# Performance work log

Hardware: AMD Instinct MI355X
Metric: run time of the kernel (lower is better)

## Reference

```python
import jax, jax.numpy as jnp
import numpy as np

H = 256        # hidden_size
HEADS = 8      # conv1 heads
B = 256        # number of graphs (sessions)
L = 64         # nodes per graph (max_length)
N = B * L      # total nodes
E = 131072     # edges before self-loops
NNODE = 37000  # item vocabulary / num classes


def setup_inputs() -> dict:
    key = jax.random.key(0)
    ks = jax.random.split(key, 16)
    s = 0.02
    return {
        "x_ids": jax.random.randint(ks[0], (N,), 0, NNODE + 1),
        "edge_index": jax.random.randint(ks[1], (2, E), 0, N),
        "batch": jnp.repeat(jnp.arange(B, dtype=jnp.int32), L),
        "emb": jax.random.normal(ks[2], (NNODE + 1, H)) * s,
        "W1": jax.random.normal(ks[3], (H, HEADS * H)) * s,
        "att_src1": jax.random.normal(ks[4], (HEADS, H)) * s,
        "att_dst1": jax.random.normal(ks[5], (HEADS, H)) * s,
        "b1": jnp.zeros((HEADS * H,)),
        "W2": jax.random.normal(ks[6], (HEADS * H, H)) * s,
        "att_src2": jax.random.normal(ks[7], (1, H)) * s,
        "att_dst2": jax.random.normal(ks[8], (1, H)) * s,
        "b2": jnp.zeros((H,)),
        "Wih": jax.random.normal(ks[9], (4 * H, H)) * s,
        "Whh": jax.random.normal(ks[10], (4 * H, H)) * s,
        "bih": jnp.zeros((4 * H,)),
        "bhh": jnp.zeros((4 * H,)),
        "Wp": jax.random.normal(ks[11], (NNODE, H)) * s,
        "bp": jnp.zeros((NNODE,)),
    }


def gat_conv(x, src, dst, W, a_src, a_dst, bias, concat):
    # PyG GATConv: linear -> per-head attention logits -> leaky_relu ->
    # segment-softmax over incoming edges per dst node -> scatter-add.
    n = x.shape[0]
    heads = a_src.shape[0]
    h = (x @ W).reshape(n, heads, -1)                       # [N, heads, out]
    alpha_s = (h * a_src).sum(-1)                            # [N, heads]
    alpha_d = (h * a_dst).sum(-1)
    e = jax.nn.leaky_relu(alpha_s[src] + alpha_d[dst], 0.2)  # [E, heads]
    m = jax.ops.segment_max(e, dst, num_segments=n)
    p = jnp.exp(e - m[dst])
    z = jax.ops.segment_sum(p, dst, num_segments=n)
    alpha = p / (z[dst] + 1e-16)                             # edge softmax
    out = jax.ops.segment_sum(alpha[:, :, None] * h[src], dst, num_segments=n)
    out = out.reshape(n, -1) if concat else out.mean(axis=1)
    return out + bias


def reference(x_ids, edge_index, batch, emb, W1, att_src1, att_dst1, b1,
              W2, att_src2, att_dst2, b2, Wih, Whh, bih, bhh, Wp, bp):
    n = x_ids.shape[0]
    # GATConv default add_self_loops=True
    loops = jnp.arange(n)
    src = jnp.concatenate([edge_index[0], loops])
    dst = jnp.concatenate([edge_index[1], loops])

    emb = emb.at[0].set(0.0)  # padding_idx=0
    x = emb[x_ids]
    # eval mode: dropout is identity
    x = jax.nn.elu(gat_conv(x, src, dst, W1, att_src1, att_dst1, b1, True))
    x = gat_conv(x, src, dst, W2, att_src2, att_dst2, b2, False)  # [N, H]

    # pack variable-length graphs into padded [B, L, H] sequences
    lengths = jax.ops.segment_sum(jnp.ones((n,), jnp.int32), batch, num_segments=B)
    starts = jnp.cumsum(lengths) - lengths
    pos = jnp.arange(n) - starts[batch]
    seq = jnp.zeros((B, L, x.shape[-1]), x.dtype).at[batch, pos].set(x)
    mask = jnp.arange(L)[None, :] < lengths[:, None]  # [B, L]

    # single-layer LSTM; masking emulates pack_padded_sequence: h_n is the
    # hidden state at each sequence's true last timestep
    def step(carry, xs):
        h_prev, c_prev = carry
        x_t, m_t = xs
        g = x_t @ Wih.T + h_prev @ Whh.T + bih + bhh
        i, f, gg, o = jnp.split(g, 4, axis=-1)
        c_new = jax.nn.sigmoid(f) * c_prev + jax.nn.sigmoid(i) * jnp.tanh(gg)
        h_new = jax.nn.sigmoid(o) * jnp.tanh(c_new)
        mm = m_t[:, None]
        return (jnp.where(mm, h_new, h_prev), jnp.where(mm, c_new, c_prev)), None

    h0 = jnp.zeros((B, x.shape[-1]), x.dtype)
    (hT, _), _ = jax.lax.scan(step, (h0, h0),
                              (seq.transpose(1, 0, 2), mask.T))
    return hT @ Wp.T + bp  # [B, NNODE] scores
```

## Files before the change

### kernel.cpp

```cpp
#include <hip/hip_runtime.h>
#include <hip/hip_bf16.h>
#include <cstdint>

#define HD 256
#define NHEADS 8
#define NB 256
#define SL 64
#define NN 16384
#define NE 131072
#define NTOT (NE + NN)

typedef float floatx4 __attribute__((ext_vector_type(4)));
typedef short shortx8 __attribute__((ext_vector_type(8)));
typedef unsigned short ushortx8 __attribute__((ext_vector_type(8)));
typedef unsigned short ushortx4 __attribute__((ext_vector_type(4)));

__device__ __forceinline__ unsigned short f2bf(float f) {
    union { float f; unsigned u; } a; a.f = f;
    unsigned r = a.u + 0x7fffu + ((a.u >> 16) & 1u);
    return (unsigned short)(r >> 16);
}
__device__ __forceinline__ float bf2f(unsigned short b) {
    union { unsigned u; float f; } a; a.u = ((unsigned)b) << 16;
    return a.f;
}

__device__ __forceinline__ void store_b16_sys(unsigned short* p, unsigned v) {
    asm volatile("global_store_short %0, %1, off sc0 sc1" :: "v"(p), "v"(v) : "memory");
}
__device__ __forceinline__ shortx8 load_b128_sys(const unsigned short* p) {
    shortx8 r;
    asm volatile("global_load_dwordx4 %0, %1, off sc0 sc1" : "=v"(r) : "v"(p) : "memory");
    return r;
}


__global__ void k_cast_bf16(const float* __restrict__ in, unsigned short* __restrict__ out, int n4) {
    int i = blockIdx.x * 256 + threadIdx.x;
    if (i >= n4) return;
    float4 v = ((const float4*)in)[i];
    ushortx4 o;
    o[0] = f2bf(v.x); o[1] = f2bf(v.y); o[2] = f2bf(v.z); o[3] = f2bf(v.w);
    *(ushortx4*)&out[i * 4] = o;
}

__global__ void k_transpose_bf16(const float* __restrict__ in, unsigned short* __restrict__ out,
                                 int K, int N) {
    __shared__ float t[32][33];
    int nb = blockIdx.x * 32, kb = blockIdx.y * 32;
    int tx = threadIdx.x, ty = threadIdx.y;
#pragma unroll
    for (int i = 0; i < 4; ++i) {
        int k = kb + ty + i * 8;
        t[ty + i * 8][tx] = in[(size_t)k * N + nb + tx];
    }
    __syncthreads();
#pragma unroll
    for (int i = 0; i < 4; ++i) {
        int nrow = nb + ty + i * 8;
        out[(size_t)nrow * K + kb + tx] = f2bf(t[tx][ty + i * 8]);
    }
}

__global__ void k_add2(const float* __restrict__ a, const float* __restrict__ b,
                       float* __restrict__ o, int n) {
    int i = blockIdx.x * 256 + threadIdx.x;
    if (i < n) o[i] = a[i] + b[i];
}

__global__ void k_zero(int* __restrict__ p, int n) {
    int i = blockIdx.x * 256 + threadIdx.x;
    if (i < n) p[i] = 0;
}

__global__ void k_gather_x(const int* __restrict__ ids, const float* __restrict__ emb,
                           unsigned short* __restrict__ xb) {
    int i = blockIdx.x * 256 + threadIdx.x;
    int n = i >> 6, d4 = (i & 63) << 2;
    int id = ids[n];
    float4 v = make_float4(0.f, 0.f, 0.f, 0.f);
    if (id != 0) v = *(const float4*)&emb[(size_t)id * HD + d4];
    ushortx4 o;
    o[0] = f2bf(v.x); o[1] = f2bf(v.y); o[2] = f2bf(v.z); o[3] = f2bf(v.w);
    *(ushortx4*)&xb[(size_t)n * HD + d4] = o;
}


template <bool OUT_BF16, bool HAS_BIAS>
__global__ __launch_bounds__(256, 2) void k_gemm_bt(
    const unsigned short* __restrict__ A, const unsigned short* __restrict__ B,
    void* __restrict__ C, const float* __restrict__ bias, int M, int Nn, int K) {
    constexpr int LDT = 56;
    __shared__ unsigned short As[128 * LDT];
    __shared__ unsigned short Bs[128 * LDT];
    int tid = threadIdx.x;
    int wave = tid >> 6, lane = tid & 63;
    int q = lane >> 4, c16 = lane & 15;
    long m0 = (long)blockIdx.x * 128;
    long n0 = (long)blockIdx.y * 128;
    int wm = (wave & 1) << 6, wn = (wave >> 1) << 6;
    floatx4 acc[4][4] = {};
    int lrow = tid >> 2;
    int lk = (tid & 3) << 3;
    const unsigned short* Arow0 = A + (m0 + lrow) * K + lk;
    const unsigned short* Arow1 = A + (m0 + 64 + lrow) * K + lk;
    long nb0 = n0 + lrow;      if (nb0 >= Nn) nb0 = Nn - 1;
    long nb1 = n0 + 64 + lrow; if (nb1 >= Nn) nb1 = Nn - 1;
    const unsigned short* Brow0 = B + nb0 * K + lk;
    const unsigned short* Brow1 = B + nb1 * K + lk;

    for (int k0 = 0; k0 < K; k0 += 32) {
        ushortx8 a0 = *(const ushortx8*)(Arow0 + k0);
        ushortx8 a1 = *(const ushortx8*)(Arow1 + k0);
        ushortx8 b0 = *(const ushortx8*)(Brow0 + k0);
        ushortx8 b1 = *(const ushortx8*)(Brow1 + k0);
        __syncthreads();
        *(ushortx8*)&As[lrow * LDT + lk] = a0;
        *(ushortx8*)&As[(64 + lrow) * LDT + lk] = a1;
        *(ushortx8*)&Bs[lrow * LDT + lk] = b0;
        *(ushortx8*)&Bs[(64 + lrow) * LDT + lk] = b1;
        __syncthreads();
        shortx8 af[4], bfr[4];
#pragma unroll
        for (int mt = 0; mt < 4; ++mt)
            af[mt] = *(const shortx8*)&As[(wm + mt * 16 + c16) * LDT + q * 8];
#pragma unroll
        for (int nt = 0; nt < 4; ++nt)
            bfr[nt] = *(const shortx8*)&Bs[(wn + nt * 16 + c16) * LDT + q * 8];
#pragma unroll
        for (int mt = 0; mt < 4; ++mt)
#pragma unroll
            for (int nt = 0; nt < 4; ++nt)
                acc[mt][nt] = __builtin_amdgcn_mfma_f32_16x16x32_bf16(af[mt], bfr[nt], acc[mt][nt], 0, 0, 0);
    }
#pragma unroll
    for (int mt = 0; mt < 4; ++mt) {
        long row_base = m0 + wm + mt * 16 + q * 4;
#pragma unroll
        for (int nt = 0; nt < 4; ++nt) {
            long col = n0 + wn + nt * 16 + c16;
            if (col >= Nn) continue;
            float bv = HAS_BIAS ? bias[col] : 0.0f;
#pragma unroll
            for (int r = 0; r < 4; ++r) {
                float v = acc[mt][nt][r] + bv;
                long idx = (row_base + r) * (long)Nn + col;
                if (OUT_BF16) ((unsigned short*)C)[idx] = f2bf(v);
                else          ((float*)C)[idx] = v;
            }
        }
    }
}


__global__ void k_alpha1(const unsigned short* __restrict__ h1b, const float* __restrict__ asrc,
                         const float* __restrict__ adst, float* __restrict__ als,
                         float* __restrict__ ald) {
    int n = blockIdx.x, t = threadIdx.x;
    ushortx8 hv = *(const ushortx8*)&h1b[(size_t)n * 2048 + t * 8];
    float s = 0.f, d = 0.f;
#pragma unroll
    for (int j = 0; j < 8; ++j) {
        float f = bf2f(hv[j]);
        s += f * asrc[t * 8 + j];
        d += f * adst[t * 8 + j];
    }
    for (int o = 16; o; o >>= 1) { s += __shfl_down(s, o, 32); d += __shfl_down(d, o, 32); }
    if ((t & 31) == 0) { als[n * 8 + (t >> 5)] = s; ald[n * 8 + (t >> 5)] = d; }
}

__global__ void k_alpha2(const unsigned short* __restrict__ x2b, const float* __restrict__ asrc,
                         const float* __restrict__ adst, float* __restrict__ als,
                         float* __restrict__ ald) {
    int n = blockIdx.x, t = threadIdx.x;
    ushortx4 hv = *(const ushortx4*)&x2b[(size_t)n * 256 + t * 4];
    float s = 0.f, d = 0.f;
#pragma unroll
    for (int j = 0; j < 4; ++j) {
        float f = bf2f(hv[j]);
        s += f * asrc[t * 4 + j];
        d += f * adst[t * 4 + j];
    }
    for (int o = 32; o; o >>= 1) { s += __shfl_down(s, o, 64); d += __shfl_down(d, o, 64); }
    if (t == 0) { als[n] = s; ald[n] = d; }
}


__global__ void k_deg_init(int* __restrict__ deg) {
    int i = blockIdx.x * 256 + threadIdx.x;
    if (i < NN) deg[i] = 1;
}
__global__ void k_deg_count(const int* __restrict__ ei, int* __restrict__ deg) {
    int e = blockIdx.x * 256 + threadIdx.x;
    if (e < NE) atomicAdd(&deg[ei[NE + e]], 1);
}
__global__ void k_scan(const int* __restrict__ deg, int* __restrict__ row_start,
                       int* __restrict__ cursor) {
    __shared__ int s[1024];
    int t = threadIdx.x;
    int base = t * 16;
    int loc[16]; int sum = 0;
#pragma unroll
    for (int i = 0; i < 16; ++i) { loc[i] = deg[base + i]; sum += loc[i]; }
    s[t] = sum;
    __syncthreads();
    for (int o = 1; o < 1024; o <<= 1) {
        int v = (t >= o) ? s[t - o] : 0;
        __syncthreads();
        s[t] += v;
        __syncthreads();
    }
    int ex = s[t] - sum;
#pragma unroll
    for (int i = 0; i < 16; ++i) {
        row_start[base + i] = ex;
        cursor[base + i] = ex;
        ex += loc[i];
    }
    if (t == 0) row_start[NN] = NTOT;
}
__global__ void k_fill(const int* __restrict__ ei, int* __restrict__ cursor,
                       int* __restrict__ csr_src) {
    int e = blockIdx.x * 256 + threadIdx.x;
    if (e >= NTOT) return;
    int s, d;
    if (e < NE) { s = ei[e]; d = ei[NE + e]; }
    else        { s = e - NE; d = s; }
    int p = atomicAdd(&cursor[d], 1);
    csr_src[p] = s;
}


__global__ __launch_bounds__(256) void k_agg1(
    const int* __restrict__ row_start, const int* __restrict__ csr_src,
    const float* __restrict__ als, const float* __restrict__ ald,
    const unsigned short* __restrict__ h1b, const float* __restrict__ b1,
    unsigned short* __restrict__ out1b) {
    int n = blockIdx.x, t = threadIdx.x;
    int rs = row_start[n];
    int deg = row_start[n + 1] - rs;
    __shared__ float sm[8], sz[8], sad[8];
    if (t < 8) sad[t] = ald[n * 8 + t];
    __syncthreads();
    int hh = t >> 5, ii = t & 31;
    float adh = sad[hh];
    float lm = -1e30f;
    for (int i = ii; i < deg; i += 32) {
        int s = csr_src[rs + i];
        float e = als[s * 8 + hh] + adh;
        e = e >= 0.f ? e : 0.2f * e;
        lm = fmaxf(lm, e);
    }
    for (int o = 16; o; o >>= 1) lm = fmaxf(lm, __shfl_down(lm, o, 32));
    if (ii == 0) sm[hh] = lm;
    __syncthreads();
    float mh = sm[hh];
    float lz = 0.f;
    for (int i = ii; i < deg; i += 32) {
        int s = csr_src[rs + i];
        float e = als[s * 8 + hh] + adh;
        e = e >= 0.f ? e : 0.2f * e;
        lz += expf(e - mh);
    }
    for (int o = 16; o; o >>= 1) lz += __shfl_down(lz, o, 32);
    if (ii == 0) sz[hh] = lz;
    __syncthreads();
    float inv_z = 1.0f / (sz[hh] + 1e-16f);
    float acc[8] = {0.f, 0.f, 0.f, 0.f, 0.f, 0.f, 0.f, 0.f};
    for (int i = 0; i < deg; ++i) {
        int s = csr_src[rs + i];
        float e = als[s * 8 + hh] + adh;
        e = e >= 0.f ? e : 0.2f * e;
        float w = expf(e - mh) * inv_z;
        ushortx8 hv = *(const ushortx8*)&h1b[(size_t)s * 2048 + t * 8];
#pragma unroll
        for (int j = 0; j < 8; ++j) acc[j] += w * bf2f(hv[j]);
    }
    ushortx8 o8;
#pragma unroll
    for (int j = 0; j < 8; ++j) {
        float v = acc[j] + b1[t * 8 + j];
        v = v > 0.f ? v : expm1f(v);
        o8[j] = f2bf(v);
    }
    *(ushortx8*)&out1b[(size_t)n * 2048 + t * 8] = o8;
}

__global__ void k_agg2(const int* __restrict__ row_start, const int* __restrict__ csr_src,
                       const float* __restrict__ als, const float* __restrict__ ald,
                       const unsigned short* __restrict__ x2b, const float* __restrict__ b2,
                       unsigned short* __restrict__ out2b) {
    int n = blockIdx.x, t = threadIdx.x;
    int rs = row_start[n];
    int deg = row_start[n + 1] - rs;
    float adn = ald[n];
    float lm = -1e30f;
    for (int i = t; i < deg; i += 64) {
        float e = als[csr_src[rs + i]] + adn;
        e = e >= 0.f ? e : 0.2f * e;
        lm = fmaxf(lm, e);
    }
    for (int o = 32; o; o >>= 1) lm = fmaxf(lm, __shfl_down(lm, o, 64));
    float mh = __shfl(lm, 0, 64);
    float lz = 0.f;
    for (int i = t; i < deg; i += 64) {
        float e = als[csr_src[rs + i]] + adn;
        e = e >= 0.f ? e : 0.2f * e;
        lz += expf(e - mh);
    }
    for (int o = 32; o; o >>= 1) lz += __shfl_down(lz, o, 64);
    float zz = __shfl(lz, 0, 64);
    float inv_z = 1.0f / (zz + 1e-16f);
    float acc[4] = {0.f, 0.f, 0.f, 0.f};
    for (int i = 0; i < deg; ++i) {
        int s = csr_src[rs + i];
        float e = als[s] + adn;
        e = e >= 0.f ? e : 0.2f * e;
        float w = expf(e - mh) * inv_z;
        ushortx4 hv = *(const ushortx4*)&x2b[(size_t)s * 256 + t * 4];
#pragma unroll
        for (int j = 0; j < 4; ++j) acc[j] += w * bf2f(hv[j]);
    }
    ushortx4 o4;
#pragma unroll
    for (int j = 0; j < 4; ++j) o4[j] = f2bf(acc[j] + b2[t * 4 + j]);
    *(ushortx4*)&out2b[(size_t)n * 256 + t * 4] = o4;
}

__global__ void k_repack_whh(const unsigned short* __restrict__ Whhb,
                             unsigned short* __restrict__ WhhR) {
    int i = blockIdx.x * 256 + threadIdx.x;
    int lane = i & 63;
    int fi = i >> 6;
    int f = fi & 3, k0 = (fi >> 2) & 7, w = (fi >> 5) & 3, s = fi >> 7;
    int q = lane >> 4, c16 = lane & 15;
    int gcol = f * 256 + s * 64 + w * 16 + c16;
    int k = k0 * 32 + q * 8;
    ushortx8 v = *(const ushortx8*)&Whhb[(size_t)gcol * 256 + k];
    *(ushortx8*)&WhhR[(size_t)fi * 512 + lane * 8] = v;
}


__global__ __launch_bounds__(256, 1) void k_lstm8(
    const float* __restrict__ Xg, const unsigned short* __restrict__ WhhR,
    unsigned short* __restrict__ hX, int* __restrict__ flags) {
    __shared__ unsigned short wlds[4 * 32 * 512];

    int tid = threadIdx.x;
    int w = tid >> 6, lane = tid & 63;
    int q = lane >> 4, c16 = lane & 15;
    int g = blockIdx.x & 15, s = blockIdx.x >> 4;
    int scol = s * 64 + w * 16 + c16;
    const int fbase = g * 64;

    const unsigned short* wsrc = WhhR + (size_t)((s * 4 + w) * 32) * 512 + lane * 8;
#pragma unroll
    for (int fi = 0; fi < 32; ++fi)
        *(shortx8*)&wlds[(w * 32 + fi) * 512 + lane * 8] =
            *(const shortx8*)(wsrc + fi * 512);

    float cst[4] = {0.f, 0.f, 0.f, 0.f};

    for (int t = 0; t < SL; ++t) {
        float xg[4][4];
#pragma unroll
        for (int r = 0; r < 4; ++r) {
            const float* xp = Xg + ((size_t)(g * 16 + q * 4 + r) * SL + t) * 1024 + scol;
#pragma unroll
            for (int f = 0; f < 4; ++f) xg[r][f] = xp[f * 256];
        }

        floatx4 acc[4] = {};
        if (t > 0) {
            if (tid == 0) {
                int spins = 0;
                while (__hip_atomic_fetch_add(&flags[fbase + t - 1], 0, __ATOMIC_RELAXED,
                                              __HIP_MEMORY_SCOPE_AGENT) < 4) {
                    __builtin_amdgcn_s_sleep(2);
                    if (++spins > 65536) break;
                }
            }
            __syncthreads();

            const unsigned short* hp =
                hX + ((size_t)(t - 1) * 256 + g * 16 + c16) * 256 + q * 8;
            shortx8 af[8];
#pragma unroll
            for (int k0 = 0; k0 < 8; ++k0) af[k0] = load_b128_sys(hp + k0 * 32);
            asm volatile("s_waitcnt vmcnt(0)" ::: "memory");
            __builtin_amdgcn_sched_barrier(0);
#pragma unroll
            for (int k0 = 0; k0 < 8; ++k0)
#pragma unroll
                for (int f = 0; f < 4; ++f) {
                    shortx8 b = *(const shortx8*)&wlds[(w * 32 + k0 * 4 + f) * 512 + lane * 8];
                    acc[f] = __builtin_amdgcn_mfma_f32_16x16x32_bf16(af[k0], b, acc[f], 0, 0, 0);
                }
        }

        unsigned short* hw = hX + ((size_t)t * 256 + g * 16) * 256 + scol;
#pragma unroll
        for (int r = 0; r < 4; ++r) {
            float gi = acc[0][r] + xg[r][0];
            float gf = acc[1][r] + xg[r][1];
            float gG = acc[2][r] + xg[r][2];
            float go = acc[3][r] + xg[r][3];
            float si = __builtin_amdgcn_rcpf(1.f + __expf(-gi));
            float sf = __builtin_amdgcn_rcpf(1.f + __expf(-gf));
            float so = __builtin_amdgcn_rcpf(1.f + __expf(-go));
            float tg = 1.f - 2.f * __builtin_amdgcn_rcpf(1.f + __expf(2.f * gG));
            float c = sf * cst[r] + si * tg;
            cst[r] = c;
            float tc = 1.f - 2.f * __builtin_amdgcn_rcpf(1.f + __expf(2.f * c));
            store_b16_sys(hw + (q * 4 + r) * 256, (unsigned)f2bf(so * tc));
        }

        if (t < SL - 1) {
            asm volatile("s_waitcnt vmcnt(0)" ::: "memory");
            __syncthreads();
            if (tid == 0)
                __hip_atomic_fetch_add(&flags[fbase + t], 1, __ATOMIC_RELAXED,
                                       __HIP_MEMORY_SCOPE_AGENT);
        }
    }
}


extern "C" void kernel_launch(void* const* d_in, const int* in_sizes, int n_in,
                              void* d_out, int out_size, void* d_ws, size_t ws_size,
                              hipStream_t stream) {
    const int*   x_ids = (const int*)d_in[0];
    const int*   ei    = (const int*)d_in[1];
    const float* emb   = (const float*)d_in[3];
    const float* W1    = (const float*)d_in[4];
    const float* as1w  = (const float*)d_in[5];
    const float* ad1w  = (const float*)d_in[6];
    const float* b1    = (const float*)d_in[7];
    const float* W2    = (const float*)d_in[8];
    const float* as2w  = (const float*)d_in[9];
    const float* ad2w  = (const float*)d_in[10];
    const float* b2    = (const float*)d_in[11];
    const float* Wih   = (const float*)d_in[12];
    const float* Whh   = (const float*)d_in[13];
    const float* bih   = (const float*)d_in[14];
    const float* bhh   = (const float*)d_in[15];
    const float* Wp    = (const float*)d_in[16];
    const float* bp    = (const float*)d_in[17];

    char* ws = (char*)d_ws;
    size_t off = 0;
    auto alloc = [&](size_t bytes) -> void* {
        void* p = ws + off;
        off += (bytes + 255) & ~(size_t)255;
        return p;
    };
    unsigned short* h1b   = (unsigned short*)alloc((size_t)NN * 2048 * 2);
    float*          Xg    = (float*)h1b;
    unsigned short* out1b = (unsigned short*)alloc((size_t)NN * 2048 * 2);
    unsigned short* hX    = out1b;
    unsigned short* xb    = (unsigned short*)alloc((size_t)NN * 256 * 2);
    unsigned short* x2b   = (unsigned short*)alloc((size_t)NN * 256 * 2);
    unsigned short* out2b = (unsigned short*)alloc((size_t)NN * 256 * 2);
    unsigned short* W1t   = (unsigned short*)alloc((size_t)2048 * 256 * 2);
    unsigned short* W2t   = (unsigned short*)alloc((size_t)256 * 2048 * 2);
    unsigned short* Wihb  = (unsigned short*)alloc((size_t)1024 * 256 * 2);
    unsigned short* Whhb  = (unsigned short*)alloc((size_t)1024 * 256 * 2);
    unsigned short* WhhR  = (unsigned short*)alloc((size_t)1024 * 256 * 2);
    unsigned short* Wpb   = (unsigned short*)alloc((size_t)37000 * 256 * 2);
    float*          bb    = (float*)alloc(1024 * 4);
    float*          als1  = (float*)alloc((size_t)NN * 8 * 4);
    float*          ald1  = (float*)alloc((size_t)NN * 8 * 4);
    float*          als2  = (float*)alloc((size_t)NN * 4);
    float*          ald2  = (float*)alloc((size_t)NN * 4);
    int* deg       = (int*)alloc((size_t)NN * 4);
    int* row_start = (int*)alloc((size_t)(NN + 1) * 4);
    int* cursor    = (int*)alloc((size_t)NN * 4);
    int* csr_src   = (int*)alloc((size_t)NTOT * 4);
    int* flags     = (int*)alloc((size_t)16 * 64 * 4);
    (void)ws_size; (void)in_sizes; (void)n_in; (void)out_size;

    k_transpose_bf16<<<dim3(2048 / 32, 256 / 32), dim3(32, 8), 0, stream>>>(W1, W1t, 256, 2048);
    k_transpose_bf16<<<dim3(256 / 32, 2048 / 32), dim3(32, 8), 0, stream>>>(W2, W2t, 2048, 256);
    k_cast_bf16<<<(262144 / 4 + 255) / 256, 256, 0, stream>>>(Wih, Wihb, 262144 / 4);
    k_cast_bf16<<<(262144 / 4 + 255) / 256, 256, 0, stream>>>(Whh, Whhb, 262144 / 4);
    k_cast_bf16<<<(9472000 / 4 + 255) / 256, 256, 0, stream>>>(Wp, Wpb, 9472000 / 4);
    k_add2<<<4, 256, 0, stream>>>(bih, bhh, bb, 1024);
    k_repack_whh<<<32768 / 256, 256, 0, stream>>>(Whhb, WhhR);
    k_zero<<<4, 256, 0, stream>>>(flags, 1024);

    k_deg_init<<<NN / 256, 256, 0, stream>>>(deg);
    k_deg_count<<<NE / 256, 256, 0, stream>>>(ei, deg);
    k_scan<<<1, 1024, 0, stream>>>(deg, row_start, cursor);
    k_fill<<<(NTOT + 255) / 256, 256, 0, stream>>>(ei, cursor, csr_src);

    k_gather_x<<<NN * 64 / 256, 256, 0, stream>>>(x_ids, emb, xb);

    k_gemm_bt<true, false><<<dim3(NN / 128, 2048 / 128), 256, 0, stream>>>(
        xb, W1t, h1b, nullptr, NN, 2048, 256);
    k_alpha1<<<NN, 256, 0, stream>>>(h1b, as1w, ad1w, als1, ald1);
    k_agg1<<<NN, 256, 0, stream>>>(row_start, csr_src, als1, ald1, h1b, b1, out1b);

    k_gemm_bt<true, false><<<dim3(NN / 128, 256 / 128), 256, 0, stream>>>(
        out1b, W2t, x2b, nullptr, NN, 256, 2048);
    k_alpha2<<<NN, 64, 0, stream>>>(x2b, as2w, ad2w, als2, ald2);
    k_agg2<<<NN, 64, 0, stream>>>(row_start, csr_src, als2, ald2, x2b, b2, out2b);

    k_gemm_bt<false, true><<<dim3(NN / 128, 1024 / 128), 256, 0, stream>>>(
        out2b, Wihb, Xg, bb, NN, 1024, 256);
    k_lstm8<<<64, 256, 0, stream>>>(Xg, WhhR, hX, flags);

    k_gemm_bt<false, true><<<dim3(256 / 128, (37000 + 127) / 128), 256, 0, stream>>>(
        hX + (size_t)63 * 256 * 256, Wpb, (float*)d_out, bp, 256, 37000, 256);
}
```

Baseline: 649.8 us.

## Replace LSTM flag-based inter-block sync with tagged hidden-state polling

The persistent LSTM kernel no longer counts per-step flags with atomics and block barriers. Each hidden-state value is stored as a 32-bit word carrying the bf16 value plus a timestep tag, and consumer waves poll the data directly until every tag matches. This removes the atomic counter, the barrier after stores and the producer-side wait, shortening the per-step critical path across blocks. In exchange it doubles the hidden-state bytes, adds a large zero-fill of the tagged buffer, and spins on wide loads that may retry many times.

```diff
diff --git a/kernel.cpp b/kernel.cpp
--- a/kernel.cpp
+++ b/kernel.cpp
@@ -14,6 +14,7 @@
 typedef short shortx8 __attribute__((ext_vector_type(8)));
 typedef unsigned short ushortx8 __attribute__((ext_vector_type(8)));
 typedef unsigned short ushortx4 __attribute__((ext_vector_type(4)));
+typedef unsigned uintx4 __attribute__((ext_vector_type(4)));
 
 __device__ __forceinline__ unsigned short f2bf(float f) {
     union { float f; unsigned u; } a; a.f = f;
@@ -25,11 +26,11 @@
     return a.f;
 }
 
-__device__ __forceinline__ void store_b16_sys(unsigned short* p, unsigned v) {
-    asm volatile("global_store_short %0, %1, off sc0 sc1" :: "v"(p), "v"(v) : "memory");
-}
-__device__ __forceinline__ shortx8 load_b128_sys(const unsigned short* p) {
-    shortx8 r;
+__device__ __forceinline__ void store_b32_sys(unsigned* p, unsigned v) {
+    asm volatile("global_store_dword %0, %1, off sc0 sc1" :: "v"(p), "v"(v) : "memory");
+}
+__device__ __forceinline__ uintx4 load_b128_sys_u(const unsigned* p) {
+    uintx4 r;
     asm volatile("global_load_dwordx4 %0, %1, off sc0 sc1" : "=v"(r) : "v"(p) : "memory");
     return r;
 }
@@ -341,9 +342,9 @@
 }
 
 
-__global__ __launch_bounds__(256, 1) void k_lstm8(
+__global__ __launch_bounds__(256, 1) void k_lstm9(
     const float* __restrict__ Xg, const unsigned short* __restrict__ WhhR,
-    unsigned short* __restrict__ hX, int* __restrict__ flags) {
+    unsigned* __restrict__ hP, unsigned short* __restrict__ hTb) {
     __shared__ unsigned short wlds[4 * 32 * 512];
 
     int tid = threadIdx.x;
@@ -351,13 +352,13 @@
     int q = lane >> 4, c16 = lane & 15;
     int g = blockIdx.x & 15, s = blockIdx.x >> 4;
     int scol = s * 64 + w * 16 + c16;
-    const int fbase = g * 64;
 
     const unsigned short* wsrc = WhhR + (size_t)((s * 4 + w) * 32) * 512 + lane * 8;
 #pragma unroll
     for (int fi = 0; fi < 32; ++fi)
         *(shortx8*)&wlds[(w * 32 + fi) * 512 + lane * 8] =
             *(const shortx8*)(wsrc + fi * 512);
+    __syncthreads();
 
     float cst[4] = {0.f, 0.f, 0.f, 0.f};
 
@@ -372,33 +373,42 @@
 
         floatx4 acc[4] = {};
         if (t > 0) {
-            if (tid == 0) {
-                int spins = 0;
-                while (__hip_atomic_fetch_add(&flags[fbase + t - 1], 0, __ATOMIC_RELAXED,
-                                              __HIP_MEMORY_SCOPE_AGENT) < 4) {
-                    __builtin_amdgcn_s_sleep(2);
-                    if (++spins > 65536) break;
+            const unsigned* hp = hP + ((size_t)(t - 1) * 256 + g * 16 + c16) * 256;
+            unsigned tag = (unsigned)t;
+            uintx4 pk[16];
+            int tries = 0;
+            for (;;) {
+#pragma unroll
+                for (int k0 = 0; k0 < 8; ++k0)
+#pragma unroll
+                    for (int h2 = 0; h2 < 2; ++h2)
+                        pk[k0 * 2 + h2] = load_b128_sys_u(hp + k0 * 32 + q * 8 + h2 * 4);
+                asm volatile("s_waitcnt vmcnt(0)" ::: "memory");
+                bool good = true;
+#pragma unroll
+                for (int j = 0; j < 16; ++j)
+#pragma unroll
+                    for (int e = 0; e < 4; ++e) good &= ((pk[j][e] >> 16) == tag);
+                if (__all((int)good) || ++tries > 50000) break;
+                __builtin_amdgcn_s_sleep(2);
+            }
+            __builtin_amdgcn_sched_barrier(0);
+
+#pragma unroll
+            for (int k0 = 0; k0 < 8; ++k0) {
+                shortx8 a;
+#pragma unroll
+                for (int e = 0; e < 8; ++e)
+                    a[e] = (short)(pk[k0 * 2 + (e >> 2)][e & 3] & 0xffffu);
+#pragma unroll
+                for (int f = 0; f < 4; ++f) {
+                    shortx8 b = *(const shortx8*)&wlds[(w * 32 + k0 * 4 + f) * 512 + lane * 8];
+                    acc[f] = __builtin_amdgcn_mfma_f32_16x16x32_bf16(a, b, acc[f], 0, 0, 0);
                 }
             }
-            __syncthreads();
-
-            const unsigned short* hp =
-                hX + ((size_t)(t - 1) * 256 + g * 16 + c16) * 256 + q * 8;
-            shortx8 af[8];
-#pragma unroll
-            for (int k0 = 0; k0 < 8; ++k0) af[k0] = load_b128_sys(hp + k0 * 32);
-            asm volatile("s_waitcnt vmcnt(0)" ::: "memory");
-            __builtin_amdgcn_sched_barrier(0);
-#pragma unroll
-            for (int k0 = 0; k0 < 8; ++k0)
-#pragma unroll
-                for (int f = 0; f < 4; ++f) {
-                    shortx8 b = *(const shortx8*)&wlds[(w * 32 + k0 * 4 + f) * 512 + lane * 8];
-                    acc[f] = __builtin_amdgcn_mfma_f32_16x16x32_bf16(af[k0], b, acc[f], 0, 0, 0);
-                }
         }
 
-        unsigned short* hw = hX + ((size_t)t * 256 + g * 16) * 256 + scol;
+        unsigned* hw = hP + ((size_t)t * 256 + g * 16) * 256 + scol;
 #pragma unroll
         for (int r = 0; r < 4; ++r) {
             float gi = acc[0][r] + xg[r][0];
@@ -412,15 +422,12 @@
             float c = sf * cst[r] + si * tg;
             cst[r] = c;
             float tc = 1.f - 2.f * __builtin_amdgcn_rcpf(1.f + __expf(2.f * c));
-            store_b16_sys(hw + (q * 4 + r) * 256, (unsigned)f2bf(so * tc));
-        }
-
-        if (t < SL - 1) {
-            asm volatile("s_waitcnt vmcnt(0)" ::: "memory");
-            __syncthreads();
-            if (tid == 0)
-                __hip_atomic_fetch_add(&flags[fbase + t], 1, __ATOMIC_RELAXED,
-                                       __HIP_MEMORY_SCOPE_AGENT);
+            unsigned short hv = f2bf(so * tc);
+            if (t < SL - 1)
+                store_b32_sys(hw + (q * 4 + r) * 256,
+                              (((unsigned)(t + 1)) << 16) | (unsigned)hv);
+            else
+                hTb[(size_t)(g * 16 + q * 4 + r) * 256 + scol] = hv;
         }
     }
 }
@@ -457,7 +464,6 @@
     unsigned short* h1b   = (unsigned short*)alloc((size_t)NN * 2048 * 2);
     float*          Xg    = (float*)h1b;
     unsigned short* out1b = (unsigned short*)alloc((size_t)NN * 2048 * 2);
-    unsigned short* hX    = out1b;
     unsigned short* xb    = (unsigned short*)alloc((size_t)NN * 256 * 2);
     unsigned short* x2b   = (unsigned short*)alloc((size_t)NN * 256 * 2);
     unsigned short* out2b = (unsigned short*)alloc((size_t)NN * 256 * 2);
@@ -472,11 +478,12 @@
     float*          ald1  = (float*)alloc((size_t)NN * 8 * 4);
     float*          als2  = (float*)alloc((size_t)NN * 4);
     float*          ald2  = (float*)alloc((size_t)NN * 4);
+    unsigned*       hP    = (unsigned*)alloc((size_t)SL * 256 * 256 * 4);
+    unsigned short* hTb   = (unsigned short*)alloc((size_t)256 * 256 * 2);
     int* deg       = (int*)alloc((size_t)NN * 4);
     int* row_start = (int*)alloc((size_t)(NN + 1) * 4);
     int* cursor    = (int*)alloc((size_t)NN * 4);
     int* csr_src   = (int*)alloc((size_t)NTOT * 4);
-    int* flags     = (int*)alloc((size_t)16 * 64 * 4);
     (void)ws_size; (void)in_sizes; (void)n_in; (void)out_size;
 
     k_transpose_bf16<<<dim3(2048 / 32, 256 / 32), dim3(32, 8), 0, stream>>>(W1, W1t, 256, 2048);
@@ -486,7 +493,7 @@
     k_cast_bf16<<<(9472000 / 4 + 255) / 256, 256, 0, stream>>>(Wp, Wpb, 9472000 / 4);
     k_add2<<<4, 256, 0, stream>>>(bih, bhh, bb, 1024);
     k_repack_whh<<<32768 / 256, 256, 0, stream>>>(Whhb, WhhR);
-    k_zero<<<4, 256, 0, stream>>>(flags, 1024);
+    k_zero<<<(SL * 256 * 256) / 256, 256, 0, stream>>>((int*)hP, SL * 256 * 256);
 
     k_deg_init<<<NN / 256, 256, 0, stream>>>(deg);
     k_deg_count<<<NE / 256, 256, 0, stream>>>(ei, deg);
@@ -507,8 +514,8 @@
 
     k_gemm_bt<false, true><<<dim3(NN / 128, 1024 / 128), 256, 0, stream>>>(
         out2b, Wihb, Xg, bb, NN, 1024, 256);
-    k_lstm8<<<64, 256, 0, stream>>>(Xg, WhhR, hX, flags);
+    k_lstm9<<<64, 256, 0, stream>>>(Xg, WhhR, hP, hTb);
 
     k_gemm_bt<false, true><<<dim3(256 / 128, (37000 + 127) / 128), 256, 0, stream>>>(
-        hX + (size_t)63 * 256 * 256, Wpb, (float*)d_out, bp, 256, 37000, 256);
-}
+        hTb, Wpb, (float*)d_out, bp, 256, 37000, 256);
+}
```

Measured after the change: 790.1 us. +21.6%, slower.

## Reorder GAT layer 1 to aggregate raw embeddings before the projection

Applied to the files above, without the earlier changes.

Layer-1 attention logits are now taken from a small GEMM of x against precomputed vectors V = W1·a, so the full 2048-wide h1 is never needed for them. The kernel then aggregates the 256-wide input features per head (k_aggx) instead of gathering 2048-wide projected rows for every edge. A per-head batched GEMM (k_gemm_b8) projects the aggregated features with W1 and fuses the bias add and ELU. This swaps a heavy edge-wise gather of h1 for an 8x larger intermediate buffer plus a per-head GEMM, and the bf16 rounding now happens at different points than before.

```diff
diff --git a/kernel.cpp b/kernel.cpp
--- a/kernel.cpp
+++ b/kernel.cpp
@@ -152,22 +152,85 @@
     }
 }
 
-
-__global__ void k_alpha1(const unsigned short* __restrict__ h1b, const float* __restrict__ asrc,
-                         const float* __restrict__ adst, float* __restrict__ als,
-                         float* __restrict__ ald) {
-    int n = blockIdx.x, t = threadIdx.x;
-    ushortx8 hv = *(const ushortx8*)&h1b[(size_t)n * 2048 + t * 8];
-    float s = 0.f, d = 0.f;
-#pragma unroll
-    for (int j = 0; j < 8; ++j) {
-        float f = bf2f(hv[j]);
-        s += f * asrc[t * 8 + j];
-        d += f * adst[t * 8 + j];
-    }
-    for (int o = 16; o; o >>= 1) { s += __shfl_down(s, o, 32); d += __shfl_down(d, o, 32); }
-    if ((t & 31) == 0) { als[n * 8 + (t >> 5)] = s; ald[n * 8 + (t >> 5)] = d; }
-}
+__global__ __launch_bounds__(256, 2) void k_gemm_b8(
+    const unsigned short* __restrict__ Ab, const unsigned short* __restrict__ W1t,
+    unsigned short* __restrict__ C, const float* __restrict__ b1) {
+    constexpr int LDT = 56;
+    __shared__ unsigned short As[128 * LDT];
+    __shared__ unsigned short Bs[128 * LDT];
+    int tid = threadIdx.x;
+    int wave = tid >> 6, lane = tid & 63;
+    int q = lane >> 4, c16 = lane & 15;
+    int hh = blockIdx.z;
+    const unsigned short* A = Ab + (size_t)hh * NN * 256;
+    const unsigned short* B = W1t + (size_t)hh * 256 * 256;
+    long m0 = (long)blockIdx.x * 128;
+    long n0 = (long)blockIdx.y * 128;
+    int wm = (wave & 1) << 6, wn = (wave >> 1) << 6;
+    floatx4 acc[4][4] = {};
+    int lrow = tid >> 2;
+    int lk = (tid & 3) << 3;
+    const unsigned short* Arow0 = A + (m0 + lrow) * 256 + lk;
+    const unsigned short* Arow1 = A + (m0 + 64 + lrow) * 256 + lk;
+    const unsigned short* Brow0 = B + (n0 + lrow) * 256 + lk;
+    const unsigned short* Brow1 = B + (n0 + 64 + lrow) * 256 + lk;
+
+    for (int k0 = 0; k0 < 256; k0 += 32) {
+        ushortx8 a0 = *(const ushortx8*)(Arow0 + k0);
+        ushortx8 a1 = *(const ushortx8*)(Arow1 + k0);
+        ushortx8 b0 = *(const ushortx8*)(Brow0 + k0);
+        ushortx8 b1 = *(const ushortx8*)(Brow1 + k0);
+        __syncthreads();
+        *(ushortx8*)&As[lrow * LDT + lk] = a0;
+        *(ushortx8*)&As[(64 + lrow) * LDT + lk] = a1;
+        *(ushortx8*)&Bs[lrow * LDT + lk] = b0;
+        *(ushortx8*)&Bs[(64 + lrow) * LDT + lk] = b1;
+        __syncthreads();
+        shortx8 af[4], bfr[4];
+#pragma unroll
+        for (int mt = 0; mt < 4; ++mt)
+            af[mt] = *(const shortx8*)&As[(wm + mt * 16 + c16) * LDT + q * 8];
+#pragma unroll
+        for (int nt = 0; nt < 4; ++nt)
+            bfr[nt] = *(const shortx8*)&Bs[(wn + nt * 16 + c16) * LDT + q * 8];
+#pragma unroll
+        for (int mt = 0; mt < 4; ++mt)
+#pragma unroll
+            for (int nt = 0; nt < 4; ++nt)
+                acc[mt][nt] = __builtin_amdgcn_mfma_f32_16x16x32_bf16(af[mt], bfr[nt], acc[mt][nt], 0, 0, 0);
+    }
+#pragma unroll
+    for (int mt = 0; mt < 4; ++mt) {
+        long row_base = m0 + wm + mt * 16 + q * 4;
+#pragma unroll
+        for (int nt = 0; nt < 4; ++nt) {
+            int gcol = hh * 256 + (int)(n0 + wn + nt * 16 + c16);
+            float bv = b1[gcol];
+#pragma unroll
+            for (int r = 0; r < 4; ++r) {
+                float v = acc[mt][nt][r] + bv;
+                v = v > 0.f ? v : expm1f(v);
+                C[(row_base + r) * 2048 + gcol] = f2bf(v);
+            }
+        }
+    }
+}
+
+__global__ void k_build_v(const float* __restrict__ W1, const float* __restrict__ as1,
+                          const float* __restrict__ ad1, unsigned short* __restrict__ Vb) {
+    __shared__ float av[256];
+    int o = blockIdx.x, k = threadIdx.x;
+    int hh = o & 7;
+    const float* a = (o < 8) ? as1 : ad1;
+    av[k] = a[hh * 256 + k];
+    __syncthreads();
+    const float* wrow = W1 + (size_t)k * 2048 + hh * 256;
+    float sum = 0.f;
+#pragma unroll 8
+    for (int d = 0; d < 256; ++d) sum += wrow[d] * av[d];
+    Vb[o * 256 + k] = f2bf(sum);
+}
+
 
 __global__ void k_alpha2(const unsigned short* __restrict__ x2b, const float* __restrict__ asrc,
                          const float* __restrict__ adst, float* __restrict__ als,
@@ -230,24 +293,24 @@
     csr_src[p] = s;
 }
 
-
-__global__ __launch_bounds__(256) void k_agg1(
+__global__ __launch_bounds__(256) void k_aggx(
     const int* __restrict__ row_start, const int* __restrict__ csr_src,
-    const float* __restrict__ als, const float* __restrict__ ald,
-    const unsigned short* __restrict__ h1b, const float* __restrict__ b1,
-    unsigned short* __restrict__ out1b) {
+    const float* __restrict__ D, const unsigned short* __restrict__ xb,
+    unsigned short* __restrict__ aggxb) {
     int n = blockIdx.x, t = threadIdx.x;
     int rs = row_start[n];
     int deg = row_start[n + 1] - rs;
-    __shared__ float sm[8], sz[8], sad[8];
-    if (t < 8) sad[t] = ald[n * 8 + t];
+    __shared__ float sad[8], sm[8], sinvz[8];
+    __shared__ int sed[32];
+    __shared__ float wlds[32][8];
+    if (t < 8) sad[t] = D[n * 16 + 8 + t];
     __syncthreads();
     int hh = t >> 5, ii = t & 31;
     float adh = sad[hh];
     float lm = -1e30f;
     for (int i = ii; i < deg; i += 32) {
         int s = csr_src[rs + i];
-        float e = als[s * 8 + hh] + adh;
+        float e = D[s * 16 + hh] + adh;
         e = e >= 0.f ? e : 0.2f * e;
         lm = fmaxf(lm, e);
     }
@@ -258,33 +321,39 @@
     float lz = 0.f;
     for (int i = ii; i < deg; i += 32) {
         int s = csr_src[rs + i];
-        float e = als[s * 8 + hh] + adh;
+        float e = D[s * 16 + hh] + adh;
         e = e >= 0.f ? e : 0.2f * e;
         lz += expf(e - mh);
     }
     for (int o = 16; o; o >>= 1) lz += __shfl_down(lz, o, 32);
-    if (ii == 0) sz[hh] = lz;
+    if (ii == 0) sinvz[hh] = 1.0f / (lz + 1e-16f);
     __syncthreads();
-    float inv_z = 1.0f / (sz[hh] + 1e-16f);
+
     float acc[8] = {0.f, 0.f, 0.f, 0.f, 0.f, 0.f, 0.f, 0.f};
-    for (int i = 0; i < deg; ++i) {
-        int s = csr_src[rs + i];
-        float e = als[s * 8 + hh] + adh;
-        e = e >= 0.f ? e : 0.2f * e;
-        float w = expf(e - mh) * inv_z;
-        ushortx8 hv = *(const ushortx8*)&h1b[(size_t)s * 2048 + t * 8];
-#pragma unroll
-        for (int j = 0; j < 8; ++j) acc[j] += w * bf2f(hv[j]);
-    }
-    ushortx8 o8;
-#pragma unroll
-    for (int j = 0; j < 8; ++j) {
-        float v = acc[j] + b1[t * 8 + j];
-        v = v > 0.f ? v : expm1f(v);
-        o8[j] = f2bf(v);
-    }
-    *(ushortx8*)&out1b[(size_t)n * 2048 + t * 8] = o8;
-}
+    int eh = t & 7, ee = t >> 3;
+    for (int base = 0; base < deg; base += 32) {
+        int cnt = min(32, deg - base);
+        if (t < 32) sed[t] = (t < cnt) ? csr_src[rs + base + t] : 0;
+        __syncthreads();
+        if (ee < cnt) {
+            int s = sed[ee];
+            float e = D[s * 16 + eh] + sad[eh];
+            e = e >= 0.f ? e : 0.2f * e;
+            wlds[ee][eh] = expf(e - sm[eh]) * sinvz[eh];
+        }
+        __syncthreads();
+        for (int e = 0; e < cnt; ++e) {
+            float xv = bf2f(xb[(size_t)sed[e] * 256 + t]);
+#pragma unroll
+            for (int h = 0; h < 8; ++h) acc[h] += wlds[e][h] * xv;
+        }
+        __syncthreads();
+    }
+#pragma unroll
+    for (int h = 0; h < 8; ++h)
+        aggxb[((size_t)h * NN + n) * 256 + t] = f2bf(acc[h]);
+}
+
 
 __global__ void k_agg2(const int* __restrict__ row_start, const int* __restrict__ csr_src,
                        const float* __restrict__ als, const float* __restrict__ ald,
@@ -454,8 +523,9 @@
         off += (bytes + 255) & ~(size_t)255;
         return p;
     };
-    unsigned short* h1b   = (unsigned short*)alloc((size_t)NN * 2048 * 2);
-    float*          Xg    = (float*)h1b;
+    unsigned short* U     = (unsigned short*)alloc((size_t)8 * NN * 256 * 2);
+    unsigned short* aggxb = U;
+    float*          Xg    = (float*)U;
     unsigned short* out1b = (unsigned short*)alloc((size_t)NN * 2048 * 2);
     unsigned short* hX    = out1b;
     unsigned short* xb    = (unsigned short*)alloc((size_t)NN * 256 * 2);
@@ -467,17 +537,18 @@
     unsigned short* Whhb  = (unsigned short*)alloc((size_t)1024 * 256 * 2);
     unsigned short* WhhR  = (unsigned short*)alloc((size_t)1024 * 256 * 2);
     unsigned short* Wpb   = (unsigned short*)alloc((size_t)37000 * 256 * 2);
+    unsigned short* Vb    = (unsigned short*)alloc((size_t)16 * 256 * 2);
     float*          bb    = (float*)alloc(1024 * 4);
-    float*          als1  = (float*)alloc((size_t)NN * 8 * 4);
-    float*          ald1  = (float*)alloc((size_t)NN * 8 * 4);
+    float*          D     = (float*)alloc((size_t)NN * 16 * 4);
     float*          als2  = (float*)alloc((size_t)NN * 4);
     float*          ald2  = (float*)alloc((size_t)NN * 4);
+    unsigned short* hTb   = (unsigned short*)alloc((size_t)256 * 256 * 2);
     int* deg       = (int*)alloc((size_t)NN * 4);
     int* row_start = (int*)alloc((size_t)(NN + 1) * 4);
     int* cursor    = (int*)alloc((size_t)NN * 4);
     int* csr_src   = (int*)alloc((size_t)NTOT * 4);
     int* flags     = (int*)alloc((size_t)16 * 64 * 4);
-    (void)ws_size; (void)in_sizes; (void)n_in; (void)out_size;
+    (void)ws_size; (void)in_sizes; (void)n_in; (void)out_size; (void)hTb;
 
     k_transpose_bf16<<<dim3(2048 / 32, 256 / 32), dim3(32, 8), 0, stream>>>(W1, W1t, 256, 2048);
     k_transpose_bf16<<<dim3(256 / 32, 2048 / 32), dim3(32, 8), 0, stream>>>(W2, W2t, 2048, 256);
@@ -487,6 +558,7 @@
     k_add2<<<4, 256, 0, stream>>>(bih, bhh, bb, 1024);
     k_repack_whh<<<32768 / 256, 256, 0, stream>>>(Whhb, WhhR);
     k_zero<<<4, 256, 0, stream>>>(flags, 1024);
+    k_build_v<<<16, 256, 0, stream>>>(W1, as1w, ad1w, Vb);
 
     k_deg_init<<<NN / 256, 256, 0, stream>>>(deg);
     k_deg_count<<<NE / 256, 256, 0, stream>>>(ei, deg);
@@ -495,10 +567,10 @@
 
     k_gather_x<<<NN * 64 / 256, 256, 0, stream>>>(x_ids, emb, xb);
 
-    k_gemm_bt<true, false><<<dim3(NN / 128, 2048 / 128), 256, 0, stream>>>(
-        xb, W1t, h1b, nullptr, NN, 2048, 256);
-    k_alpha1<<<NN, 256, 0, stream>>>(h1b, as1w, ad1w, als1, ald1);
-    k_agg1<<<NN, 256, 0, stream>>>(row_start, csr_src, als1, ald1, h1b, b1, out1b);
+    k_gemm_bt<false, false><<<dim3(NN / 128, 1), 256, 0, stream>>>(
+        xb, Vb, D, nullptr, NN, 16, 256);
+    k_aggx<<<NN, 256, 0, stream>>>(row_start, csr_src, D, xb, aggxb);
+    k_gemm_b8<<<dim3(NN / 128, 2, 8), 256, 0, stream>>>(aggxb, W1t, out1b, b1);
 
     k_gemm_bt<true, false><<<dim3(NN / 128, 256 / 128), 256, 0, stream>>>(
         out1b, W2t, x2b, nullptr, NN, 256, 2048);
```

Result: faster. 618.4 us (-4.8%).
